# Kernel tuning notes

Hardware: AMD Instinct MI355X
Metric: run time of the kernel (lower is better)

## Reference

```python
import jax, jax.numpy as jnp
import numpy as np

SAMPLE_RATE = 4096.0  # matches init_kwargs sample_rate
STATE_DIM = 64
LENGTH, CHANNELS = 8192, 512


def setup_inputs() -> dict:
    key = jax.random.key(0)
    kx, kc = jax.random.split(key)
    x = jax.random.normal(kx, (LENGTH, CHANNELS), dtype=jnp.float32)
    # param init exactly as in the flax module
    logA = jnp.log(1.0 + jnp.arange(STATE_DIM, dtype=jnp.float32))
    B = jnp.ones((STATE_DIM,), dtype=jnp.float32)
    C = 0.01 * jax.random.normal(kc, (STATE_DIM,), dtype=jnp.float32)  # nn.initializers.normal() stddev=0.01
    return {"x": x, "logA": logA, "B": B, "C": C}


def reference(x, logA, B, C):
    # ZOH-style discretization: A = -exp(logA); Abar = exp(A*dt); Bbar = (Abar-1)*B/A
    dt = 1.0 / SAMPLE_RATE
    A = -jnp.exp(logA)                # (N,)
    Abar = jnp.exp(A * dt)            # (N,)
    Bbar = (Abar - 1.0) * B / A       # (N,)

    channels = x.shape[1]
    h0 = jnp.zeros((channels, logA.shape[0]), dtype=x.dtype)  # (C, N)

    def step(h, xt):
        # h: (C, N), xt: (C,)
        h = Abar[None, :] * h + xt[:, None] * Bbar[None, :]
        y = h @ C                      # (C,)
        return h, y

    _, y = jax.lax.scan(step, h0, x)   # y: (L, C)
    return y
```

## Files before the change

### kernel.cpp

```cpp
#include <hip/hip_runtime.h>
#include <math.h>

#define LENGTH   8192
#define CHANNELS 512
#define NSTATE   64
#define TCHUNK   64
#define NCHUNK   (LENGTH / TCHUNK)
#define E_ELEMS  (NCHUNK * NSTATE * CHANNELS)
#define LOG2E    1.4426950408889634f
#define DT       (1.0f / 4096.0f)


__global__ __launch_bounds__(256, 4) void k_pass1(const float* __restrict__ x,
                                                  const float* __restrict__ logA,
                                                  float* __restrict__ E) {
    __shared__ float Xl[64 * 64];
    __shared__ float Gl[64 * 64];
    __shared__ float l2ab[64];
    int tid = threadIdx.x;
    int k   = blockIdx.x >> 3;
    int c0g = (blockIdx.x & 7) * 64;

    if (tid < 64) {
        float A = -expf(logA[tid]);
        l2ab[tid] = A * DT * LOG2E;
    }
    const float* xsrc = x + (size_t)k * TCHUNK * CHANNELS + c0g;
    #pragma unroll
    for (int i = 0; i < 4; ++i) {
        int idx = tid + 256 * i;
        int s = idx >> 4, cq = (idx & 15) * 4;
        *(float4*)&Xl[s * 64 + cq] = *(const float4*)(xsrc + (size_t)s * CHANNELS + cq);
    }
    __syncthreads();
    {
        int s = tid >> 2, nb = (tid & 3) * 16;
        float e = (float)(63 - s);
        #pragma unroll
        for (int j = 0; j < 16; ++j) Gl[s * 64 + nb + j] = exp2f(e * l2ab[nb + j]);
    }
    __syncthreads();

    int c0 = (tid & 15) * 4;
    int n0 = (tid >> 4) * 4;
    float a00=0,a01=0,a02=0,a03=0, a10=0,a11=0,a12=0,a13=0;
    float a20=0,a21=0,a22=0,a23=0, a30=0,a31=0,a32=0,a33=0;

    #pragma unroll 8
    for (int s = 0; s < 64; ++s) {
        float4 xv = *(const float4*)&Xl[s * 64 + c0];
        float4 gv = *(const float4*)&Gl[s * 64 + n0];
        a00 = fmaf(gv.x, xv.x, a00); a01 = fmaf(gv.x, xv.y, a01);
        a02 = fmaf(gv.x, xv.z, a02); a03 = fmaf(gv.x, xv.w, a03);
        a10 = fmaf(gv.y, xv.x, a10); a11 = fmaf(gv.y, xv.y, a11);
        a12 = fmaf(gv.y, xv.z, a12); a13 = fmaf(gv.y, xv.w, a13);
        a20 = fmaf(gv.z, xv.x, a20); a21 = fmaf(gv.z, xv.y, a21);
        a22 = fmaf(gv.z, xv.z, a22); a23 = fmaf(gv.z, xv.w, a23);
        a30 = fmaf(gv.w, xv.x, a30); a31 = fmaf(gv.w, xv.y, a31);
        a32 = fmaf(gv.w, xv.z, a32); a33 = fmaf(gv.w, xv.w, a33);
    }

    float* Ep = E + ((size_t)k * NSTATE + n0) * CHANNELS + c0g + c0;
    *(float4*)(Ep)                    = make_float4(a00, a01, a02, a03);
    *(float4*)(Ep + 1 * CHANNELS)     = make_float4(a10, a11, a12, a13);
    *(float4*)(Ep + 2 * CHANNELS)     = make_float4(a20, a21, a22, a23);
    *(float4*)(Ep + 3 * CHANNELS)     = make_float4(a30, a31, a32, a33);
}

#define G2 16
__global__ __launch_bounds__(64, 1) void k_pass2(float* __restrict__ W,
                                                 const float* __restrict__ logA) {
    int gtid = blockIdx.x * 64 + threadIdx.x;
    int c = gtid & (CHANNELS - 1);
    int n = gtid >> 9;
    float A  = -expf(logA[n]);
    float aT = exp2f(A * (64.0f * DT) * LOG2E);
    float* p = W + (size_t)n * CHANNELS + c;
    const size_t S = (size_t)NSTATE * CHANNELS;

    float e[2][G2];
    #pragma unroll
    for (int j = 0; j < G2; ++j) e[0][j] = p[(size_t)j * S];

    float hc = 0.f;
    #pragma unroll
    for (int k0 = 0; k0 < NCHUNK; k0 += G2) {
        const int cur = (k0 / G2) & 1;
        const int nxt = cur ^ 1;
        if (k0 + G2 < NCHUNK) {
            #pragma unroll
            for (int j = 0; j < G2; ++j) e[nxt][j] = p[(size_t)(k0 + G2 + j) * S];
        }
        #pragma unroll
        for (int j = 0; j < G2; ++j) {
            p[(size_t)(k0 + j) * S] = hc;
            hc = fmaf(aT, hc, e[cur][j]);
        }
    }
}

__global__ __launch_bounds__(256, 2) void k_pass3(const float* __restrict__ x,
                                                  const float* __restrict__ logA,
                                                  const float* __restrict__ Bv,
                                                  const float* __restrict__ Cv,
                                                  const float* __restrict__ Wc,
                                                  float* __restrict__ y) {
    __shared__ float Xl[64 * 64];
    __shared__ float Hl[64 * 64];
    __shared__ float Tl[64 * 64];
    __shared__ float Pl[64 * 64];
    __shared__ float l2ab[64], CBl[64], Kl[64], Kpart[4 * 64];
    int tid = threadIdx.x;
    int k   = blockIdx.x >> 3;
    int c0g = (blockIdx.x & 7) * 64;

    if (tid < 64) {
        int n = tid;
        float A    = -expf(logA[n]);
        float Bbar = expm1f(A * DT) * Bv[n] / A;
        l2ab[n] = A * DT * LOG2E;
        CBl[n]  = Cv[n] * Bbar;
    }
    const float* xsrc = x  + (size_t)k * TCHUNK * CHANNELS + c0g;
    const float* hsrc = Wc + (size_t)k * NSTATE * CHANNELS + c0g;
    #pragma unroll
    for (int i = 0; i < 4; ++i) {
        int idx = tid + 256 * i;
        int s = idx >> 4, cq = (idx & 15) * 4;
        *(float4*)&Xl[s * 64 + cq] = *(const float4*)(xsrc + (size_t)s * CHANNELS + cq);
        *(float4*)&Hl[s * 64 + cq] = *(const float4*)(hsrc + (size_t)s * CHANNELS + cq);
    }
    __syncthreads();
    {
        int n = tid >> 2, tb = (tid & 3) * 16;
        float l2 = l2ab[n], cb = CBl[n];
        #pragma unroll
        for (int j = 0; j < 16; ++j)
            Pl[n * 64 + tb + j] = cb * exp2f((float)(tb + j + 1) * l2);
    }
    {
        int d = tid & 63, q = tid >> 6;
        float s = 0.f;
        #pragma unroll
        for (int i = 0; i < 16; ++i) {
            int n = q * 16 + i;
            s = fmaf(CBl[n], exp2f((float)d * l2ab[n]), s);
        }
        Kpart[q * 64 + d] = s;
    }
    __syncthreads();
    if (tid < 64)
        Kl[tid] = (Kpart[tid] + Kpart[64 + tid]) + (Kpart[128 + tid] + Kpart[192 + tid]);
    __syncthreads();
    {
        int s = tid >> 2, tb = (tid & 3) * 16;
        #pragma unroll
        for (int j = 0; j < 16; ++j) {
            int t = tb + j;
            Tl[s * 64 + t] = (t >= s) ? Kl[t - s] : 0.f;
        }
    }
    __syncthreads();

    int c0 = (tid & 15) * 4;
    int t0 = (tid >> 4) * 4;
    float a00=0,a01=0,a02=0,a03=0, a10=0,a11=0,a12=0,a13=0;
    float a20=0,a21=0,a22=0,a23=0, a30=0,a31=0,a32=0,a33=0;

    #pragma unroll 4
    for (int s = 0; s < 64; ++s) {
        float4 xv = *(const float4*)&Xl[s * 64 + c0];
        float4 tv = *(const float4*)&Tl[s * 64 + t0];
        a00 = fmaf(tv.x, xv.x, a00); a01 = fmaf(tv.x, xv.y, a01);
        a02 = fmaf(tv.x, xv.z, a02); a03 = fmaf(tv.x, xv.w, a03);
        a10 = fmaf(tv.y, xv.x, a10); a11 = fmaf(tv.y, xv.y, a11);
        a12 = fmaf(tv.y, xv.z, a12); a13 = fmaf(tv.y, xv.w, a13);
        a20 = fmaf(tv.z, xv.x, a20); a21 = fmaf(tv.z, xv.y, a21);
        a22 = fmaf(tv.z, xv.z, a22); a23 = fmaf(tv.z, xv.w, a23);
        a30 = fmaf(tv.w, xv.x, a30); a31 = fmaf(tv.w, xv.y, a31);
        a32 = fmaf(tv.w, xv.z, a32); a33 = fmaf(tv.w, xv.w, a33);
    }
    #pragma unroll 4
    for (int n = 0; n < 64; ++n) {
        float4 hv = *(const float4*)&Hl[n * 64 + c0];
        float4 pv = *(const float4*)&Pl[n * 64 + t0];
        a00 = fmaf(pv.x, hv.x, a00); a01 = fmaf(pv.x, hv.y, a01);
        a02 = fmaf(pv.x, hv.z, a02); a03 = fmaf(pv.x, hv.w, a03);
        a10 = fmaf(pv.y, hv.x, a10); a11 = fmaf(pv.y, hv.y, a11);
        a12 = fmaf(pv.y, hv.z, a12); a13 = fmaf(pv.y, hv.w, a13);
        a20 = fmaf(pv.z, hv.x, a20); a21 = fmaf(pv.z, hv.y, a21);
        a22 = fmaf(pv.z, hv.z, a22); a23 = fmaf(pv.z, hv.w, a23);
        a30 = fmaf(pv.w, hv.x, a30); a31 = fmaf(pv.w, hv.y, a31);
        a32 = fmaf(pv.w, hv.z, a32); a33 = fmaf(pv.w, hv.w, a33);
    }

    float* yp = y + ((size_t)k * TCHUNK + t0) * CHANNELS + c0g + c0;
    *(float4*)(yp)                = make_float4(a00, a01, a02, a03);
    *(float4*)(yp + 1 * CHANNELS) = make_float4(a10, a11, a12, a13);
    *(float4*)(yp + 2 * CHANNELS) = make_float4(a20, a21, a22, a23);
    *(float4*)(yp + 3 * CHANNELS) = make_float4(a30, a31, a32, a33);
}

__global__ __launch_bounds__(256) void k_fallback(const float* __restrict__ x,
                                                  const float* __restrict__ logA,
                                                  const float* __restrict__ B,
                                                  const float* __restrict__ C,
                                                  float* __restrict__ y) {
    int c = blockIdx.x * blockDim.x + threadIdx.x;
    if (c >= CHANNELS) return;
    float Abar[NSTATE], CB[NSTATE], h[NSTATE];
    for (int n = 0; n < NSTATE; ++n) {
        float A    = -expf(logA[n]);
        float ab   = exp2f(A * DT * LOG2E);
        float Bbar = expm1f(A * DT) * B[n] / A;
        Abar[n] = ab;
        CB[n]   = C[n] * Bbar;
        h[n]    = 0.f;
    }
    for (int t = 0; t < LENGTH; ++t) {
        float xv = x[(size_t)t * CHANNELS + c];
        float acc = 0.f;
        for (int n = 0; n < NSTATE; ++n) {
            h[n] = fmaf(Abar[n], h[n], xv);
            acc  = fmaf(CB[n], h[n], acc);
        }
        y[(size_t)t * CHANNELS + c] = acc;
    }
}

extern "C" void kernel_launch(void* const* d_in, const int* in_sizes, int n_in,
                              void* d_out, int out_size, void* d_ws, size_t ws_size,
                              hipStream_t stream) {
    const float* x    = (const float*)d_in[0];
    const float* logA = (const float*)d_in[1];
    const float* B    = (const float*)d_in[2];
    const float* C    = (const float*)d_in[3];
    float* yout = (float*)d_out;

    if (ws_size < (size_t)E_ELEMS * sizeof(float)) {
        k_fallback<<<(CHANNELS + 255) / 256, 256, 0, stream>>>(x, logA, B, C, yout);
        return;
    }
    float* W = (float*)d_ws;

    k_pass1<<<NCHUNK * 8, 256, 0, stream>>>(x, logA, W);
    k_pass2<<<(NSTATE * CHANNELS) / 64, 64, 0, stream>>>(W, logA);
    k_pass3<<<NCHUNK * 8, 256, 0, stream>>>(x, logA, B, C, W, yout);
}
```

Measured before the change: 109.2 us.

## Replace chunk matmuls with register-resident per-thread recurrences and alias workspace to output

```diff
diff --git a/kernel.cpp b/kernel.cpp
--- a/kernel.cpp
+++ b/kernel.cpp
@@ -6,65 +6,50 @@
 #define NSTATE   64
 #define TCHUNK   64
 #define NCHUNK   (LENGTH / TCHUNK)
-#define E_ELEMS  (NCHUNK * NSTATE * CHANNELS)
 #define LOG2E    1.4426950408889634f
 #define DT       (1.0f / 4096.0f)
 
 
-__global__ __launch_bounds__(256, 4) void k_pass1(const float* __restrict__ x,
+__device__ __forceinline__ float lane_bcast_f(float v, int lane) {
+    return __int_as_float(__builtin_amdgcn_readlane(__float_as_int(v), lane));
+}
+
+__global__ __launch_bounds__(256, 2) void k_pass1(const float* __restrict__ x,
                                                   const float* __restrict__ logA,
                                                   float* __restrict__ E) {
-    __shared__ float Xl[64 * 64];
-    __shared__ float Gl[64 * 64];
-    __shared__ float l2ab[64];
-    int tid = threadIdx.x;
-    int k   = blockIdx.x >> 3;
-    int c0g = (blockIdx.x & 7) * 64;
+    int tid  = threadIdx.x;
+    int k    = blockIdx.x >> 2;
+    int c    = ((blockIdx.x & 3) << 7) + (tid & 127);
+    int half = tid >> 7;
+    int lane = tid & 63;
 
-    if (tid < 64) {
-        float A = -expf(logA[tid]);
-        l2ab[tid] = A * DT * LOG2E;
+    int   nme = (half << 5) + (lane & 31);
+    float Av  = -expf(logA[nme]);
+    float abv = exp2f(Av * DT * LOG2E);
+
+    float a[32];
+    #pragma unroll
+    for (int i = 0; i < 32; ++i) a[i] = lane_bcast_f(abv, i);
+
+    float h[32];
+    #pragma unroll
+    for (int i = 0; i < 32; ++i) h[i] = 0.f;
+
+    const float* xp = x + (size_t)k * TCHUNK * CHANNELS + c;
+    float xv = xp[0];
+    #pragma unroll 7
+    for (int t = 0; t < TCHUNK - 1; ++t) {
+        float xn = xp[(size_t)(t + 1) * CHANNELS];
+        #pragma unroll
+        for (int i = 0; i < 32; ++i) h[i] = fmaf(a[i], h[i], xv);
+        xv = xn;
     }
-    const float* xsrc = x + (size_t)k * TCHUNK * CHANNELS + c0g;
     #pragma unroll
-    for (int i = 0; i < 4; ++i) {
-        int idx = tid + 256 * i;
-        int s = idx >> 4, cq = (idx & 15) * 4;
-        *(float4*)&Xl[s * 64 + cq] = *(const float4*)(xsrc + (size_t)s * CHANNELS + cq);
-    }
-    __syncthreads();
-    {
-        int s = tid >> 2, nb = (tid & 3) * 16;
-        float e = (float)(63 - s);
-        #pragma unroll
-        for (int j = 0; j < 16; ++j) Gl[s * 64 + nb + j] = exp2f(e * l2ab[nb + j]);
-    }
-    __syncthreads();
+    for (int i = 0; i < 32; ++i) h[i] = fmaf(a[i], h[i], xv);
 
-    int c0 = (tid & 15) * 4;
-    int n0 = (tid >> 4) * 4;
-    float a00=0,a01=0,a02=0,a03=0, a10=0,a11=0,a12=0,a13=0;
-    float a20=0,a21=0,a22=0,a23=0, a30=0,a31=0,a32=0,a33=0;
-
-    #pragma unroll 8
-    for (int s = 0; s < 64; ++s) {
-        float4 xv = *(const float4*)&Xl[s * 64 + c0];
-        float4 gv = *(const float4*)&Gl[s * 64 + n0];
-        a00 = fmaf(gv.x, xv.x, a00); a01 = fmaf(gv.x, xv.y, a01);
-        a02 = fmaf(gv.x, xv.z, a02); a03 = fmaf(gv.x, xv.w, a03);
-        a10 = fmaf(gv.y, xv.x, a10); a11 = fmaf(gv.y, xv.y, a11);
-        a12 = fmaf(gv.y, xv.z, a12); a13 = fmaf(gv.y, xv.w, a13);
-        a20 = fmaf(gv.z, xv.x, a20); a21 = fmaf(gv.z, xv.y, a21);
-        a22 = fmaf(gv.z, xv.z, a22); a23 = fmaf(gv.z, xv.w, a23);
-        a30 = fmaf(gv.w, xv.x, a30); a31 = fmaf(gv.w, xv.y, a31);
-        a32 = fmaf(gv.w, xv.z, a32); a33 = fmaf(gv.w, xv.w, a33);
-    }
-
-    float* Ep = E + ((size_t)k * NSTATE + n0) * CHANNELS + c0g + c0;
-    *(float4*)(Ep)                    = make_float4(a00, a01, a02, a03);
-    *(float4*)(Ep + 1 * CHANNELS)     = make_float4(a10, a11, a12, a13);
-    *(float4*)(Ep + 2 * CHANNELS)     = make_float4(a20, a21, a22, a23);
-    *(float4*)(Ep + 3 * CHANNELS)     = make_float4(a30, a31, a32, a33);
+    float* Ep = E + ((size_t)k * NSTATE + (half << 5)) * CHANNELS + c;
+    #pragma unroll
+    for (int i = 0; i < 32; ++i) Ep[(size_t)i * CHANNELS] = h[i];
 }
 
 #define G2 16
@@ -103,128 +88,76 @@
                                                   const float* __restrict__ logA,
                                                   const float* __restrict__ Bv,
                                                   const float* __restrict__ Cv,
-                                                  const float* __restrict__ Wc,
+                                                  const float* __restrict__ W,
                                                   float* __restrict__ y) {
-    __shared__ float Xl[64 * 64];
-    __shared__ float Hl[64 * 64];
-    __shared__ float Tl[64 * 64];
-    __shared__ float Pl[64 * 64];
-    __shared__ float l2ab[64], CBl[64], Kl[64], Kpart[4 * 64];
-    int tid = threadIdx.x;
-    int k   = blockIdx.x >> 3;
-    int c0g = (blockIdx.x & 7) * 64;
+    __shared__ float yp[2][TCHUNK][128];
+    int tid  = threadIdx.x;
+    int k    = blockIdx.x >> 2;
+    int c0g  = (blockIdx.x & 3) << 7;
+    int cl   = tid & 127;
+    int c    = c0g + cl;
+    int half = tid >> 7;
+    int lane = tid & 63;
 
-    if (tid < 64) {
-        int n = tid;
-        float A    = -expf(logA[n]);
-        float Bbar = expm1f(A * DT) * Bv[n] / A;
-        l2ab[n] = A * DT * LOG2E;
-        CBl[n]  = Cv[n] * Bbar;
+    int   nme  = (half << 5) + (lane & 31);
+    float Av   = -expf(logA[nme]);
+    float abv  = exp2f(Av * DT * LOG2E);
+    float Bbar = expm1f(Av * DT) * Bv[nme] / Av;
+    float cbv  = Cv[nme] * Bbar;
+
+    float a[32], cb[32];
+    #pragma unroll
+    for (int i = 0; i < 32; ++i) {
+        a[i]  = lane_bcast_f(abv, i);
+        cb[i] = lane_bcast_f(cbv, i);
     }
-    const float* xsrc = x  + (size_t)k * TCHUNK * CHANNELS + c0g;
-    const float* hsrc = Wc + (size_t)k * NSTATE * CHANNELS + c0g;
+
+    const float* Wp = W + ((size_t)k * NSTATE + (half << 5)) * CHANNELS + c;
+    float h[32];
     #pragma unroll
-    for (int i = 0; i < 4; ++i) {
-        int idx = tid + 256 * i;
-        int s = idx >> 4, cq = (idx & 15) * 4;
-        *(float4*)&Xl[s * 64 + cq] = *(const float4*)(xsrc + (size_t)s * CHANNELS + cq);
-        *(float4*)&Hl[s * 64 + cq] = *(const float4*)(hsrc + (size_t)s * CHANNELS + cq);
-    }
-    __syncthreads();
-    {
-        int n = tid >> 2, tb = (tid & 3) * 16;
-        float l2 = l2ab[n], cb = CBl[n];
+    for (int i = 0; i < 32; ++i) h[i] = Wp[(size_t)i * CHANNELS];
+
+    const float* xp = x + (size_t)k * TCHUNK * CHANNELS + c;
+    float* ypb = &yp[half][0][cl];
+
+    float xv = xp[0];
+    #pragma unroll 3
+    for (int t = 0; t < TCHUNK - 1; ++t) {
+        float xn = xp[(size_t)(t + 1) * CHANNELS];
+        float y0 = 0.f, y1 = 0.f, y2 = 0.f, y3 = 0.f;
         #pragma unroll
-        for (int j = 0; j < 16; ++j)
-            Pl[n * 64 + tb + j] = cb * exp2f((float)(tb + j + 1) * l2);
+        for (int i = 0; i < 32; i += 4) {
+            h[i]   = fmaf(a[i],   h[i],   xv);  y0 = fmaf(cb[i],   h[i],   y0);
+            h[i+1] = fmaf(a[i+1], h[i+1], xv);  y1 = fmaf(cb[i+1], h[i+1], y1);
+            h[i+2] = fmaf(a[i+2], h[i+2], xv);  y2 = fmaf(cb[i+2], h[i+2], y2);
+            h[i+3] = fmaf(a[i+3], h[i+3], xv);  y3 = fmaf(cb[i+3], h[i+3], y3);
+        }
+        ypb[t * 128] = (y0 + y1) + (y2 + y3);
+        xv = xn;
     }
     {
-        int d = tid & 63, q = tid >> 6;
-        float s = 0.f;
+        float y0 = 0.f, y1 = 0.f, y2 = 0.f, y3 = 0.f;
         #pragma unroll
-        for (int i = 0; i < 16; ++i) {
-            int n = q * 16 + i;
-            s = fmaf(CBl[n], exp2f((float)d * l2ab[n]), s);
+        for (int i = 0; i < 32; i += 4) {
+            h[i]   = fmaf(a[i],   h[i],   xv);  y0 = fmaf(cb[i],   h[i],   y0);
+            h[i+1] = fmaf(a[i+1], h[i+1], xv);  y1 = fmaf(cb[i+1], h[i+1], y1);
+            h[i+2] = fmaf(a[i+2], h[i+2], xv);  y2 = fmaf(cb[i+2], h[i+2], y2);
+            h[i+3] = fmaf(a[i+3], h[i+3], xv);  y3 = fmaf(cb[i+3], h[i+3], y3);
         }
-        Kpart[q * 64 + d] = s;
-    }
-    __syncthreads();
-    if (tid < 64)
-        Kl[tid] = (Kpart[tid] + Kpart[64 + tid]) + (Kpart[128 + tid] + Kpart[192 + tid]);
-    __syncthreads();
-    {
-        int s = tid >> 2, tb = (tid & 3) * 16;
-        #pragma unroll
-        for (int j = 0; j < 16; ++j) {
-            int t = tb + j;
-            Tl[s * 64 + t] = (t >= s) ? Kl[t - s] : 0.f;
-        }
+        ypb[(TCHUNK - 1) * 128] = (y0 + y1) + (y2 + y3);
     }
     __syncthreads();
 
-    int c0 = (tid & 15) * 4;
-    int t0 = (tid >> 4) * 4;
-    float a00=0,a01=0,a02=0,a03=0, a10=0,a11=0,a12=0,a13=0;
-    float a20=0,a21=0,a22=0,a23=0, a30=0,a31=0,a32=0,a33=0;
-
-    #pragma unroll 4
-    for (int s = 0; s < 64; ++s) {
-        float4 xv = *(const float4*)&Xl[s * 64 + c0];
-        float4 tv = *(const float4*)&Tl[s * 64 + t0];
-        a00 = fmaf(tv.x, xv.x, a00); a01 = fmaf(tv.x, xv.y, a01);
-        a02 = fmaf(tv.x, xv.z, a02); a03 = fmaf(tv.x, xv.w, a03);
-        a10 = fmaf(tv.y, xv.x, a10); a11 = fmaf(tv.y, xv.y, a11);
-        a12 = fmaf(tv.y, xv.z, a12); a13 = fmaf(tv.y, xv.w, a13);
-        a20 = fmaf(tv.z, xv.x, a20); a21 = fmaf(tv.z, xv.y, a21);
-        a22 = fmaf(tv.z, xv.z, a22); a23 = fmaf(tv.z, xv.w, a23);
-        a30 = fmaf(tv.w, xv.x, a30); a31 = fmaf(tv.w, xv.y, a31);
-        a32 = fmaf(tv.w, xv.z, a32); a33 = fmaf(tv.w, xv.w, a33);
-    }
-    #pragma unroll 4
-    for (int n = 0; n < 64; ++n) {
-        float4 hv = *(const float4*)&Hl[n * 64 + c0];
-        float4 pv = *(const float4*)&Pl[n * 64 + t0];
-        a00 = fmaf(pv.x, hv.x, a00); a01 = fmaf(pv.x, hv.y, a01);
-        a02 = fmaf(pv.x, hv.z, a02); a03 = fmaf(pv.x, hv.w, a03);
-        a10 = fmaf(pv.y, hv.x, a10); a11 = fmaf(pv.y, hv.y, a11);
-        a12 = fmaf(pv.y, hv.z, a12); a13 = fmaf(pv.y, hv.w, a13);
-        a20 = fmaf(pv.z, hv.x, a20); a21 = fmaf(pv.z, hv.y, a21);
-        a22 = fmaf(pv.z, hv.z, a22); a23 = fmaf(pv.z, hv.w, a23);
-        a30 = fmaf(pv.w, hv.x, a30); a31 = fmaf(pv.w, hv.y, a31);
-        a32 = fmaf(pv.w, hv.z, a32); a33 = fmaf(pv.w, hv.w, a33);
-    }
-
-    float* yp = y + ((size_t)k * TCHUNK + t0) * CHANNELS + c0g + c0;
-    *(float4*)(yp)                = make_float4(a00, a01, a02, a03);
-    *(float4*)(yp + 1 * CHANNELS) = make_float4(a10, a11, a12, a13);
-    *(float4*)(yp + 2 * CHANNELS) = make_float4(a20, a21, a22, a23);
-    *(float4*)(yp + 3 * CHANNELS) = make_float4(a30, a31, a32, a33);
-}
-
-__global__ __launch_bounds__(256) void k_fallback(const float* __restrict__ x,
-                                                  const float* __restrict__ logA,
-                                                  const float* __restrict__ B,
-                                                  const float* __restrict__ C,
-                                                  float* __restrict__ y) {
-    int c = blockIdx.x * blockDim.x + threadIdx.x;
-    if (c >= CHANNELS) return;
-    float Abar[NSTATE], CB[NSTATE], h[NSTATE];
-    for (int n = 0; n < NSTATE; ++n) {
-        float A    = -expf(logA[n]);
-        float ab   = exp2f(A * DT * LOG2E);
-        float Bbar = expm1f(A * DT) * B[n] / A;
-        Abar[n] = ab;
-        CB[n]   = C[n] * Bbar;
-        h[n]    = 0.f;
-    }
-    for (int t = 0; t < LENGTH; ++t) {
-        float xv = x[(size_t)t * CHANNELS + c];
-        float acc = 0.f;
-        for (int n = 0; n < NSTATE; ++n) {
-            h[n] = fmaf(Abar[n], h[n], xv);
-            acc  = fmaf(CB[n], h[n], acc);
-        }
-        y[(size_t)t * CHANNELS + c] = acc;
+    float* yg = y + (size_t)k * TCHUNK * CHANNELS + c0g;
+    #pragma unroll
+    for (int i = 0; i < 8; ++i) {
+        int idx = (i << 8) + tid;
+        int t   = idx >> 5;
+        int cq  = (idx & 31) << 2;
+        float4 v0 = *(const float4*)&yp[0][t][cq];
+        float4 v1 = *(const float4*)&yp[1][t][cq];
+        *(float4*)(yg + (size_t)t * CHANNELS + cq) =
+            make_float4(v0.x + v1.x, v0.y + v1.y, v0.z + v1.z, v0.w + v1.w);
     }
 }
 
@@ -237,13 +170,10 @@
     const float* C    = (const float*)d_in[3];
     float* yout = (float*)d_out;
 
-    if (ws_size < (size_t)E_ELEMS * sizeof(float)) {
-        k_fallback<<<(CHANNELS + 255) / 256, 256, 0, stream>>>(x, logA, B, C, yout);
-        return;
-    }
-    float* W = (float*)d_ws;
+    float* W = yout;
+    (void)d_ws; (void)ws_size;
 
-    k_pass1<<<NCHUNK * 8, 256, 0, stream>>>(x, logA, W);
+    k_pass1<<<NCHUNK * 4, 256, 0, stream>>>(x, logA, W);
     k_pass2<<<(NSTATE * CHANNELS) / 64, 64, 0, stream>>>(W, logA);
-    k_pass3<<<NCHUNK * 8, 256, 0, stream>>>(x, logA, B, C, W, yout);
+    k_pass3<<<NCHUNK * 4, 256, 0, stream>>>(x, logA, B, C, W, yout);
 }
```

Result: faster. 103.2 us (-5.5%).
